# Performance work log

Measured on AMD Instinct MI355X. Metric: run time of the kernel, lower is better.

The kernel has to match this reference:

```python
import jax, jax.numpy as jnp
import numpy as np

D = 768; HID = 384; B = 256; T = 96
N_EMO = 128; N_CAU = 256; CK = 4; NK = N_CAU // CK; POS = 50
EPS_BN = 1e-5

def _lrelu(x):
    return jax.nn.leaky_relu(x, 0.01)

def _lstm(x, Wih, Whh, bih, bhh):
    # x: [B,T,D] -> hidden states [B,T,HID]; PyTorch gate order i,f,g,o
    h0 = jnp.zeros((x.shape[0], Whh.shape[1]), x.dtype)
    def step(carry, xt):
        h, c = carry
        g = xt @ Wih.T + bih + h @ Whh.T + bhh
        i, f, gg, o = jnp.split(g, 4, axis=-1)
        c = jax.nn.sigmoid(f) * c + jax.nn.sigmoid(i) * jnp.tanh(gg)
        h = jax.nn.sigmoid(o) * jnp.tanh(c)
        return (h, c), h
    _, hs = jax.lax.scan(step, (h0, h0), jnp.swapaxes(x, 0, 1))
    return jnp.swapaxes(hs, 0, 1)

def _item_att(E, Y):
    # E: [e,d], Y: [e,k,d] -> cat(x.repeat, y, ||x-y||, x*y) : [e,k,3d+1]
    Eb = jnp.broadcast_to(E[:, None, :], Y.shape)
    nrm = jnp.linalg.norm(Eb - Y, axis=-1, keepdims=True)
    return jnp.concatenate([Eb, Y, nrm, Eb * Y], axis=-1)

def _bn(x):
    # BatchNorm1d(affine=False, track_running_stats=False): batch stats, biased var
    m = x.mean(axis=1, keepdims=True)
    v = x.var(axis=1, keepdims=True)
    return (x - m) / jnp.sqrt(v + EPS_BN)

def setup_inputs() -> dict:
    key = jax.random.key(0)
    ks = jax.random.split(key, 26)
    s = 0.05
    g = lambda k, shp: (jax.random.normal(k, shp, jnp.float32) * s)
    inp = {
        'word_encode': jax.random.normal(ks[0], (B, T, D), jnp.float32),
        'pos_encode': jax.random.normal(ks[1], (N_EMO, NK, POS), jnp.float32),
        'dis_encode': jax.random.normal(ks[2], (1, N_CAU, POS), jnp.float32),
        'Wih_f': g(ks[3], (4 * HID, D)), 'Whh_f': g(ks[4], (4 * HID, HID)),
        'bih_f': g(ks[5], (4 * HID,)), 'bhh_f': g(ks[6], (4 * HID,)),
        'Wih_b': g(ks[7], (4 * HID, D)), 'Whh_b': g(ks[8], (4 * HID, HID)),
        'bih_b': g(ks[9], (4 * HID,)), 'bhh_b': g(ks[10], (4 * HID,)),
        's1_W': g(ks[11], (D, D)), 's1_b': g(ks[12], (D,)),
        's2_W': g(ks[13], (D, 1)),
        'rep_W': g(ks[14], (D, D)), 'rep_b': g(ks[15], (D,)),
        'W2_W': g(ks[16], (3 * D + 1 + POS, D)), 'W2_b': g(ks[17], (D,)),
        'Wo_W': g(ks[18], (D, 2)), 'Wo_b': g(ks[19], (2,)),
        'W3_W': g(ks[20], (3 * D + 2 + POS, D)), 'W3_b': g(ks[21], (D,)),
        'cls_W': g(ks[22], (D, 2)), 'cls_b': g(ks[23], (2,)),
        'sen_lengths': jax.random.randint(ks[24], (B,), T // 2, T + 1),
        'emo_idx': jnp.arange(N_EMO) * 2,
        'cau_idx': jnp.arange(N_CAU),
        'label3': jax.random.randint(ks[25], (N_EMO, 3), -1, N_CAU),
    }
    return inp

def reference(word_encode, pos_encode, dis_encode, Wih_f, Whh_f, bih_f, bhh_f,
              Wih_b, Whh_b, bih_b, bhh_b, s1_W, s1_b, s2_W, rep_W, rep_b,
              W2_W, W2_b, Wo_W, Wo_b, W3_W, W3_b, cls_W, cls_b,
              sen_lengths, emo_idx, cau_idx, label3):
    t = jnp.arange(T)
    # reverse-within-length index for the backward LSTM direction
    rev_idx = jnp.where(t[None, :] < sen_lengths[:, None],
                        sen_lengths[:, None] - 1 - t[None, :], t[None, :])
    hs_f = _lstm(word_encode, Wih_f, Whh_f, bih_f, bhh_f)
    x_rev = jnp.take_along_axis(word_encode, rev_idx[:, :, None], axis=1)
    hs_b = jnp.take_along_axis(_lstm(x_rev, Wih_b, Whh_b, bih_b, bhh_b),
                               rev_idx[:, :, None], axis=1)
    Hs = jnp.concatenate([hs_f, hs_b], axis=-1)  # [B,T,D]
    # att_var with softmax_by_length as written (mask*score / sum)
    e = (_lrelu(Hs @ s1_W + s1_b) @ s2_W)[..., 0]  # [B,T]
    mask = (t[None, :] < sen_lengths[:, None]).astype(Hs.dtype)
    num = e * mask
    alpha = num / (jnp.sum(num, axis=-1, keepdims=True) + 1e-9)
    U = jnp.einsum('bt,btd->bd', alpha, Hs)  # [B,D]
    # share_rep=True branch
    E = _lrelu(U[emo_idx] @ rep_W + rep_b)   # [n_emo,D]
    Cu = _lrelu(U[cau_idx] @ rep_W + rep_b)  # [n_cau,D]
    C = Cu.reshape(NK, CK, D)
    # per-chunk cross attention (softmax over chunk members)
    sc = jax.nn.softmax(jnp.einsum('ed,kcd->ekc', E, C), axis=-1)
    chunkEmb = jnp.einsum('ekc,kcd->ekd', sc, C)  # [e,NK,D]
    delta = jnp.concatenate([_item_att(E, chunkEmb), pos_encode], axis=-1)
    h2 = _lrelu(_bn(delta @ W2_W + W2_b))
    out2 = jax.nn.log_softmax(h2 @ Wo_W + Wo_b, axis=-1)  # [e,NK,2]
    out_feat = jax.lax.stop_gradient(jnp.argmax(out2, axis=-1).astype(Hs.dtype))
    # phase 3: all chunks selected (ck_mask all ones)
    delta_d = _item_att(E, jnp.broadcast_to(Cu[None], (N_EMO, N_CAU, D)))
    extra = jnp.repeat(out_feat, CK, axis=1)[..., None]  # [e,n_cau,1]
    dis = jnp.broadcast_to(dis_encode[0][None], (N_EMO, N_CAU, POS))
    delta3 = jnp.concatenate([delta_d, dis, extra], axis=-1)
    h3 = _lrelu(_bn(delta3 @ W3_W + W3_b))
    p = jax.nn.log_softmax(h3 @ cls_W + cls_b, axis=-1)  # [e,n_cau,2]
    # label3_out: L_cau indicator per emotion
    valid = (label3 >= 0)[..., None].astype(p.dtype)
    L = jnp.clip(jnp.sum(jax.nn.one_hot(label3, N_CAU, dtype=p.dtype) * valid,
                         axis=1), 0.0, 1.0)
    return out2, p, L
```

## Files before the change

kernel.cpp:

```cpp
#include <hip/hip_runtime.h>
#include <cstdint>
#include <cstddef>


#define DEV __device__ __forceinline__
typedef float f32x4 __attribute__((ext_vector_type(4)));
typedef __bf16 bf16;
typedef bf16 bf16x8 __attribute__((ext_vector_type(8)));

struct G32 {
    const float* A;
    const float* B;
    float* out;
    const float* bias;
    const float* s2v;
    float* escoreP;
    int M, N, K, lda, ldb, ldc;
};

template <int EPI>
__global__ __launch_bounds__(512) void k_gemm32(G32 p) {
    __shared__ __align__(16) float As[32][132];
    __shared__ __align__(16) float Bs[32][132];
    const int tid = threadIdx.x;
    const int tx = tid & 15, ty = tid >> 4;
    const int m0 = blockIdx.y * 128, n0 = blockIdx.x * 128;
    float acc[4][8] = {};
    const int ra = tid >> 2;
    const int ka = (tid & 3) * 8;

    const float* arow = p.A + (size_t)(m0 + ra) * p.lda;
    const float* brow = p.B + (size_t)(n0 + ra) * p.ldb;

    auto load_tile = [&](int kt, float* av, float* bv) {
        const float* ap = arow + kt + ka;
#pragma unroll
        for (int q = 0; q < 8; q++) av[q] = ap[q];
        const float* bp = brow + kt + ka;
#pragma unroll
        for (int q = 0; q < 8; q++) bv[q] = bp[q];
    };

    const int nt = p.K / 32;
    float av[8], bv[8];
    load_tile(0, av, bv);
    for (int t = 0; t < nt; t++) {
        __syncthreads();
#pragma unroll
        for (int q = 0; q < 8; q++) {
            As[ka + q][ra] = av[q];
            Bs[ka + q][ra] = bv[q];
        }
        __syncthreads();
        if (t + 1 < nt) load_tile((t + 1) * 32, av, bv);
#pragma unroll
        for (int kk = 0; kk < 32; kk++) {
            float a[4], b[8];
            *(f32x4*)a = *(const f32x4*)&As[kk][ty * 4];
            *(f32x4*)b = *(const f32x4*)&Bs[kk][tx * 4];
            *(f32x4*)(b + 4) = *(const f32x4*)&Bs[kk][64 + tx * 4];
#pragma unroll
            for (int i = 0; i < 4; i++)
#pragma unroll
                for (int j = 0; j < 8; j++) acc[i][j] += a[i] * b[j];
        }
    }

    if constexpr (EPI == 3) {
#pragma unroll
        for (int i = 0; i < 4; i++) {
            float s = 0.f;
#pragma unroll
            for (int j = 0; j < 8; j++) {
                int n = n0 + ((j < 4) ? tx * 4 + j : 64 + tx * 4 + (j - 4));
                float x = acc[i][j] + p.bias[n];
                x = x > 0.f ? x : 0.01f * x;
                s += x * p.s2v[n];
            }
            s += __shfl_xor(s, 1);
            s += __shfl_xor(s, 2);
            s += __shfl_xor(s, 4);
            s += __shfl_xor(s, 8);
            if (tx == 0) {
                int m = m0 + ty * 4 + i;
                p.escoreP[(size_t)m * 6 + blockIdx.x] = s;
            }
        }
    } else {
#pragma unroll
        for (int i = 0; i < 4; i++)
#pragma unroll
            for (int j = 0; j < 8; j++) {
                int m = m0 + ty * 4 + i;
                int n = n0 + ((j < 4) ? tx * 4 + j : 64 + tx * 4 + (j - 4));
                float x = acc[i][j];
                if constexpr (EPI == 0) {
                    if (p.bias) x += p.bias[n];
                } else if constexpr (EPI == 2) {
                    x += p.bias[n];
                    x = x > 0.f ? x : 0.01f * x;
                }
                p.out[(size_t)m * p.ldc + n] = x;
            }
    }
}

struct GSP {
    const float* srcA;
    const bf16* BH;
    const bf16* BL;
    float* out;
    const float* bias;
    const float* addE;
    const float* addB;
    const float* nrm;
    const float* wn;
    const float* feat;
    const float* wx;
    const float* ce;
    const float* CuEf;
    const float* pos;
    const int* slen;
    int K, ldb, ldc, c0;
};

template <int AMODE, int EPI>
__global__ __launch_bounds__(256) void k_gemm_sp(GSP p) {
    __shared__ __align__(16) bf16 AhS[128 * 32];
    __shared__ __align__(16) bf16 AlS[128 * 32];
    __shared__ __align__(16) bf16 BhS[128 * 32];
    __shared__ __align__(16) bf16 BlS[128 * 32];
    const int tid = threadIdx.x;
    const int lane = tid & 63;
    const int w = tid >> 6;
    const int wm = w >> 1, wn_ = w & 1;
    const int m0 = blockIdx.y * 128, n0 = blockIdx.x * 128;
    const int l15 = lane & 15, lq = lane >> 4;

    f32x4 zero4 = {0.f, 0.f, 0.f, 0.f};
    f32x4 acc[4][4];
#pragma unroll
    for (int i = 0; i < 4; i++)
#pragma unroll
        for (int j = 0; j < 4; j++) acc[i][j] = zero4;

    const int c0s = tid, c1s = tid + 256;
    const int ar0 = c0s >> 2, ao0 = (c0s & 3) << 3;
    const int ar1 = c1s >> 2, ao1 = (c1s & 3) << 3;
    const int gm0 = m0 + ar0, gm1 = m0 + ar1;

    const float* arow0 = nullptr;
    const float* arow1 = nullptr;
    const float *er0 = nullptr, *cr0 = nullptr, *pr0 = nullptr;
    const float *er1 = nullptr, *cr1 = nullptr, *pr1 = nullptr;
    if constexpr (AMODE == 1 || AMODE == 3) {
        int b0 = gm0 >> 5, t0 = p.c0 + (gm0 & 31);
        int b1 = gm1 >> 5, t1 = p.c0 + (gm1 & 31);
        if constexpr (AMODE == 3) {
            int len0 = p.slen[b0], len1 = p.slen[b1];
            t0 = (t0 < len0) ? len0 - 1 - t0 : t0;
            t1 = (t1 < len1) ? len1 - 1 - t1 : t1;
        }
        arow0 = p.srcA + ((size_t)b0 * 96 + t0) * 768;
        arow1 = p.srcA + ((size_t)b1 * 96 + t1) * 768;
    } else if constexpr (AMODE == 2) {
        er0 = p.CuEf + (size_t)(256 + (gm0 >> 8)) * 768;
        cr0 = p.CuEf + (size_t)(gm0 & 255) * 768;
        er1 = p.CuEf + (size_t)(256 + (gm1 >> 8)) * 768;
        cr1 = p.CuEf + (size_t)(gm1 & 255) * 768;
    } else {
        er0 = p.CuEf + (size_t)(256 + (gm0 >> 6)) * 768;
        cr0 = p.ce + (size_t)gm0 * 768;
        pr0 = p.pos + (size_t)gm0 * 50;
        er1 = p.CuEf + (size_t)(256 + (gm1 >> 6)) * 768;
        cr1 = p.ce + (size_t)gm1 * 768;
        pr1 = p.pos + (size_t)gm1 * 50;
    }
    const bf16* bh0 = p.BH + (size_t)(n0 + ar0) * p.ldb;
    const bf16* bl0 = p.BL + (size_t)(n0 + ar0) * p.ldb;
    const bf16* bh1 = p.BH + (size_t)(n0 + ar1) * p.ldb;
    const bf16* bl1 = p.BL + (size_t)(n0 + ar1) * p.ldb;

    auto loadA = [&](int kt, int ao, const float* arow, const float* er,
                     const float* cr, const float* pr, float* a) {
        if constexpr (AMODE == 1 || AMODE == 3) {
#pragma unroll
            for (int q = 0; q < 8; q++) a[q] = arow[kt + ao + q];
        } else if constexpr (AMODE == 2) {
#pragma unroll
            for (int q = 0; q < 8; q++) a[q] = er[kt + ao + q] * cr[kt + ao + q];
        } else {
#pragma unroll
            for (int q = 0; q < 8; q++) {
                int k = kt + ao + q;
                float v;
                if (k < 768) v = cr[k];
                else if (k < 1536) v = er[k - 768] * cr[k - 768];
                else if (k < 1586) v = pr[k - 1536];
                else v = 0.f;
                a[q] = v;
            }
        }
    };

    const int nt = p.K / 32;
    float a0f[8], a1f[8];
    bf16x8 b0h, b0l, b1h, b1l;
    auto load_tile = [&](int kt) {
        loadA(kt, ao0, arow0, er0, cr0, pr0, a0f);
        loadA(kt, ao1, arow1, er1, cr1, pr1, a1f);
        b0h = *(const bf16x8*)(bh0 + kt + ao0);
        b0l = *(const bf16x8*)(bl0 + kt + ao0);
        b1h = *(const bf16x8*)(bh1 + kt + ao1);
        b1l = *(const bf16x8*)(bl1 + kt + ao1);
    };

    load_tile(0);
    for (int t = 0; t < nt; t++) {
        __syncthreads();
        {
            bf16x8 h8, l8;
#pragma unroll
            for (int q = 0; q < 8; q++) {
                bf16 h = (bf16)a0f[q];
                h8[q] = h;
                l8[q] = (bf16)(a0f[q] - (float)h);
            }
            *(bf16x8*)(AhS + (c0s << 3)) = h8;
            *(bf16x8*)(AlS + (c0s << 3)) = l8;
#pragma unroll
            for (int q = 0; q < 8; q++) {
                bf16 h = (bf16)a1f[q];
                h8[q] = h;
                l8[q] = (bf16)(a1f[q] - (float)h);
            }
            *(bf16x8*)(AhS + (c1s << 3)) = h8;
            *(bf16x8*)(AlS + (c1s << 3)) = l8;
            *(bf16x8*)(BhS + (c0s << 3)) = b0h;
            *(bf16x8*)(BlS + (c0s << 3)) = b0l;
            *(bf16x8*)(BhS + (c1s << 3)) = b1h;
            *(bf16x8*)(BlS + (c1s << 3)) = b1l;
        }
        __syncthreads();
        if (t + 1 < nt) load_tile((t + 1) * 32);

        bf16x8 ah[4], bh[4], xl[4];
#pragma unroll
        for (int i = 0; i < 4; i++) {
            ah[i] = *(const bf16x8*)(AhS + (wm * 64 + i * 16 + l15) * 32 + (lq << 3));
            bh[i] = *(const bf16x8*)(BhS + (wn_ * 64 + i * 16 + l15) * 32 + (lq << 3));
        }
#pragma unroll
        for (int i = 0; i < 4; i++)
#pragma unroll
            for (int j = 0; j < 4; j++)
                acc[i][j] = __builtin_amdgcn_mfma_f32_16x16x32_bf16(ah[i], bh[j], acc[i][j], 0, 0, 0);
#pragma unroll
        for (int i = 0; i < 4; i++)
            xl[i] = *(const bf16x8*)(AlS + (wm * 64 + i * 16 + l15) * 32 + (lq << 3));
#pragma unroll
        for (int i = 0; i < 4; i++)
#pragma unroll
            for (int j = 0; j < 4; j++)
                acc[i][j] = __builtin_amdgcn_mfma_f32_16x16x32_bf16(xl[i], bh[j], acc[i][j], 0, 0, 0);
#pragma unroll
        for (int i = 0; i < 4; i++)
            xl[i] = *(const bf16x8*)(BlS + (wn_ * 64 + i * 16 + l15) * 32 + (lq << 3));
#pragma unroll
        for (int i = 0; i < 4; i++)
#pragma unroll
            for (int j = 0; j < 4; j++)
                acc[i][j] = __builtin_amdgcn_mfma_f32_16x16x32_bf16(ah[i], xl[j], acc[i][j], 0, 0, 0);
    }

#pragma unroll
    for (int i = 0; i < 4; i++)
#pragma unroll
        for (int j = 0; j < 4; j++)
#pragma unroll
            for (int r = 0; r < 4; r++) {
                int m = m0 + wm * 64 + i * 16 + (lq << 2) + r;
                int n = n0 + wn_ * 64 + j * 16 + l15;
                float v = acc[i][j][r];
                if constexpr (EPI == 1) {
                    v += p.bias[n];
                } else if constexpr (EPI == 4) {
                    int e = m >> 6;
                    v += p.addE[(size_t)e * 768 + n] + p.nrm[m] * p.wn[n] + p.bias[n];
                } else if constexpr (EPI == 5) {
                    int e = m >> 8, jj = m & 255;
                    float ex = p.feat[e * 64 + (jj >> 2)];
                    v += p.addE[(size_t)e * 768 + n] + p.addB[(size_t)jj * 768 + n] +
                         p.nrm[m] * p.wn[n] + ex * p.wx[n];
                }
                p.out[(size_t)m * p.ldc + n] = v;
            }
}

__global__ void k_wpack(const float* __restrict__ whh, float* __restrict__ wp) {
    int idx = blockIdx.x * 256 + threadIdx.x;
    if (idx < 384 * 1536) {
        int k = idx / 1536, rem = idx - k * 1536;
        int u = rem >> 2, g = rem & 3;
        wp[idx] = whh[(size_t)(g * 384 + u) * 384 + k];
    }
}

__global__ __launch_bounds__(384) void k_lstm_rows(
    const float* __restrict__ gchF, const float* __restrict__ gchB,
    const float* __restrict__ wpF, const float* __restrict__ wpB,
    float* __restrict__ hbuf, float* __restrict__ cbuf, float* __restrict__ Hs,
    const int* __restrict__ slen, int c0) {
    __shared__ __align__(16) float hlds[4][384];
    const int tid = threadIdx.x;
    const int dir = blockIdx.x & 1;
    const int r0 = (blockIdx.x >> 1) * 4;
    const float* gch = dir ? gchB : gchF;
    const float* wp = dir ? wpB : wpF;
    float* hb = hbuf + (size_t)dir * 98304;
    float* cb = cbuf + (size_t)dir * 98304;
    const int u = tid;

    {
        int r = tid / 96, c4 = (tid - r * 96) * 4;
        *(f32x4*)&hlds[r][c4] = *(const f32x4*)&hb[(size_t)(r0 + r) * 384 + c4];
    }
    float c_[4];
    int len_[4];
#pragma unroll
    for (int r = 0; r < 4; r++) {
        c_[r] = cb[(size_t)(r0 + r) * 384 + u];
        len_[r] = slen[r0 + r];
    }
    __syncthreads();

    const float* wpb = wp + (size_t)u * 4;
    for (int t = c0; t < c0 + 32; t++) {
        float acc[4][4] = {};
#pragma unroll 4
        for (int k = 0; k < 384; k++) {
            f32x4 wv = *(const f32x4*)(wpb + (size_t)k * 1536);
            float h0 = hlds[0][k], h1 = hlds[1][k];
            float h2 = hlds[2][k], h3 = hlds[3][k];
#pragma unroll
            for (int g = 0; g < 4; g++) {
                acc[0][g] += h0 * wv[g];
                acc[1][g] += h1 * wv[g];
                acc[2][g] += h2 * wv[g];
                acc[3][g] += h3 * wv[g];
            }
        }
        __syncthreads();
#pragma unroll
        for (int r = 0; r < 4; r++) {
            int bg = r0 + r;
            int len = len_[r];
            int tsrc = dir ? (t < len ? len - 1 - t : t) : t;
            const float* gp = gch + (((size_t)bg << 5) + (t & 31)) * 1536;
            float gi = acc[r][0] + gp[u];
            float gf = acc[r][1] + gp[384 + u];
            float gg2 = acc[r][2] + gp[768 + u];
            float go = acc[r][3] + gp[1152 + u];
            float si = 1.f / (1.f + __expf(-gi));
            float sf = 1.f / (1.f + __expf(-gf));
            float so = 1.f / (1.f + __expf(-go));
            float tg = tanhf(gg2);
            float cn = sf * c_[r] + si * tg;
            float hn = so * tanhf(cn);
            c_[r] = cn;
            hlds[r][u] = hn;
            int tpos = dir ? tsrc : t;
            Hs[((size_t)bg * 96 + tpos) * 768 + dir * 384 + u] = hn;
        }
        __syncthreads();
    }

    {
        int r = tid / 96, c4 = (tid - r * 96) * 4;
        *(f32x4*)&hb[(size_t)(r0 + r) * 384 + c4] = *(const f32x4*)&hlds[r][c4];
    }
#pragma unroll
    for (int r = 0; r < 4; r++) cb[(size_t)(r0 + r) * 384 + u] = c_[r];
}

__global__ void k_bias2(const float* a, const float* b, float* o, int n) {
    int i = blockIdx.x * 256 + threadIdx.x;
    if (i < n) o[i] = a[i] + b[i];
}

__global__ void k_splitw(const float* __restrict__ src, bf16* __restrict__ hi,
                         bf16* __restrict__ lo, int n) {
    int i = blockIdx.x * 256 + threadIdx.x;
    if (i < n) {
        float v = src[i];
        bf16 h = (bf16)v;
        hi[i] = h;
        lo[i] = (bf16)(v - (float)h);
    }
}

__global__ __launch_bounds__(256) void k_transp32(const float* __restrict__ src,
                                                  float* __restrict__ dst, int roff) {
    __shared__ float tile[32][33];
    int tx = threadIdx.x & 31, ty = threadIdx.x >> 5;
    int n0 = blockIdx.x * 32, k0 = blockIdx.y * 32;
#pragma unroll
    for (int r = ty; r < 32; r += 8)
        tile[r][tx] = src[(size_t)(roff + k0 + r) * 768 + n0 + tx];
    __syncthreads();
#pragma unroll
    for (int r = ty; r < 32; r += 8)
        dst[(size_t)(n0 + r) * 768 + k0 + tx] = tile[tx][r];
}

__global__ __launch_bounds__(256) void k_transp_sp(const float* __restrict__ src,
                                                   bf16* __restrict__ hi,
                                                   bf16* __restrict__ lo, int roff) {
    __shared__ float tile[32][33];
    int tx = threadIdx.x & 31, ty = threadIdx.x >> 5;
    int n0 = blockIdx.x * 32, k0 = blockIdx.y * 32;
#pragma unroll
    for (int r = ty; r < 32; r += 8)
        tile[r][tx] = src[(size_t)(roff + k0 + r) * 768 + n0 + tx];
    __syncthreads();
#pragma unroll
    for (int r = ty; r < 32; r += 8) {
        float v = tile[tx][r];
        bf16 h = (bf16)v;
        hi[(size_t)(n0 + r) * 768 + k0 + tx] = h;
        lo[(size_t)(n0 + r) * 768 + k0 + tx] = (bf16)(v - (float)h);
    }
}

__global__ __launch_bounds__(256) void k_b2cat_sp(const float* __restrict__ W2,
                                                  bf16* __restrict__ hi,
                                                  bf16* __restrict__ lo) {
    __shared__ float tile[32][33];
    int tx = threadIdx.x & 31, ty = threadIdx.x >> 5;
    int n0 = blockIdx.x * 32, k0 = blockIdx.y * 32;
#pragma unroll
    for (int r = ty; r < 32; r += 8) {
        int k = k0 + r;
        float v = 0.f;
        if (k < 1586) {
            int sr = (k < 768) ? 768 + k : 769 + k;
            v = W2[(size_t)sr * 768 + n0 + tx];
        }
        tile[r][tx] = v;
    }
    __syncthreads();
#pragma unroll
    for (int r = ty; r < 32; r += 8) {
        float v = tile[tx][r];
        bf16 h = (bf16)v;
        hi[(size_t)(n0 + r) * 1600 + k0 + tx] = h;
        lo[(size_t)(n0 + r) * 1600 + k0 + tx] = (bf16)(v - (float)h);
    }
}

__global__ __launch_bounds__(256) void k_alpha_u(const float* __restrict__ escoreP,
                                                 const float* __restrict__ Hs,
                                                 const int* __restrict__ slen,
                                                 float* __restrict__ U) {
    __shared__ float al[96];
    __shared__ float dsh;
    int b = blockIdx.x, tid = threadIdx.x;
    int len = slen[b];
    if (tid < 96) {
        const float* ep = escoreP + (size_t)(b * 96 + tid) * 6;
        float e = ep[0] + ep[1] + ep[2] + ep[3] + ep[4] + ep[5];
        al[tid] = (tid < len) ? e : 0.f;
    }
    __syncthreads();
    if (tid == 0) {
        float s = 0.f;
        for (int i = 0; i < 96; i++) s += al[i];
        dsh = 1.f / (s + 1e-9f);
    }
    __syncthreads();
    float dinv = dsh;
    for (int d = tid; d < 768; d += 256) {
        float acc = 0.f;
        const float* hp = Hs + (size_t)b * 96 * 768 + d;
        for (int tt = 0; tt < 96; tt++) acc += al[tt] * hp[(size_t)tt * 768];
        U[(size_t)b * 768 + d] = acc * dinv;
    }
}

__global__ void k_ucat(const float* __restrict__ U, const int* __restrict__ cau,
                       const int* __restrict__ emo, float* __restrict__ Ucat) {
    int i = blockIdx.x * 256 + threadIdx.x;
    if (i < 384 * 768) {
        int r = i / 768, d = i - r * 768;
        int src = (r < 256) ? cau[r] : emo[r - 256];
        Ucat[i] = U[(size_t)src * 768 + d];
    }
}

__global__ __launch_bounds__(256) void k_chunk_sc(const float* __restrict__ CuEf,
                                                  float* __restrict__ sc) {
    int m = blockIdx.x;
    int e = m >> 6, nk = m & 63;
    int tid = threadIdx.x, w = tid >> 6, lane = tid & 63;
    const float* Er = CuEf + (size_t)(256 + e) * 768;
    const float* Cr = CuEf + (size_t)(nk * 4 + w) * 768;
    float acc = 0.f;
    for (int q = lane; q < 768; q += 64) acc += Er[q] * Cr[q];
    for (int off = 32; off; off >>= 1) acc += __shfl_xor(acc, off);
    __shared__ float S[4];
    if (lane == 0) S[w] = acc;
    __syncthreads();
    if (tid == 0) {
        float mx = fmaxf(fmaxf(S[0], S[1]), fmaxf(S[2], S[3]));
        float e0 = expf(S[0] - mx), e1 = expf(S[1] - mx), e2 = expf(S[2] - mx),
              e3 = expf(S[3] - mx);
        float inv = 1.f / (e0 + e1 + e2 + e3);
        sc[4 * m] = e0 * inv; sc[4 * m + 1] = e1 * inv;
        sc[4 * m + 2] = e2 * inv; sc[4 * m + 3] = e3 * inv;
    }
}

__global__ void k_chunk_emb(const float* __restrict__ sc, const float* __restrict__ CuEf,
                            float* __restrict__ ce) {
    int i = blockIdx.x * 256 + threadIdx.x;
    if (i < 8192 * 768) {
        int m = i / 768, d = i - m * 768;
        int nk = m & 63;
        const float* base = CuEf + (size_t)(nk * 4) * 768 + d;
        ce[i] = sc[4 * m] * base[0] + sc[4 * m + 1] * base[768] +
                sc[4 * m + 2] * base[1536] + sc[4 * m + 3] * base[2304];
    }
}

__global__ __launch_bounds__(256) void k_nrm2(const float* __restrict__ ce,
                                              const float* __restrict__ CuEf,
                                              float* __restrict__ nrm2) {
    int m = blockIdx.x, tid = threadIdx.x;
    int e = m >> 6;
    const float* cr = ce + (size_t)m * 768;
    const float* er = CuEf + (size_t)(256 + e) * 768;
    float ss = 0.f;
    for (int d = tid; d < 768; d += 256) {
        float df = er[d] - cr[d];
        ss += df * df;
    }
    for (int off = 32; off; off >>= 1) ss += __shfl_xor(ss, off);
    __shared__ float red[4];
    if ((tid & 63) == 0) red[tid >> 6] = ss;
    __syncthreads();
    if (tid == 0) nrm2[m] = sqrtf(red[0] + red[1] + red[2] + red[3]);
}

__global__ __launch_bounds__(256) void k_nrm3(const float* __restrict__ CuEf,
                                              float* __restrict__ nrm3) {
    int m = blockIdx.x, tid = threadIdx.x;
    int e = m >> 8, j = m & 255;
    const float* cu = CuEf + (size_t)j * 768;
    const float* er = CuEf + (size_t)(256 + e) * 768;
    float ss = 0.f;
    for (int d = tid; d < 768; d += 256) {
        float df = er[d] - cu[d];
        ss += df * df;
    }
    for (int off = 32; off; off >>= 1) ss += __shfl_xor(ss, off);
    __shared__ float red[4];
    if ((tid & 63) == 0) red[tid >> 6] = ss;
    __syncthreads();
    if (tid == 0) nrm3[m] = sqrtf(red[0] + red[1] + red[2] + red[3]);
}

__global__ void k_bv3_dis(float* __restrict__ Bv3, const float* __restrict__ dis,
                          const float* __restrict__ W3, const float* __restrict__ b3) {
    int i = blockIdx.x * 256 + threadIdx.x;
    if (i < 256 * 768) {
        int j = i / 768, n = i - j * 768;
        float s = Bv3[i] + b3[n];
        const float* dr = dis + j * 50;
#pragma unroll 10
        for (int q = 0; q < 50; q++) s += dr[q] * W3[(size_t)(2305 + q) * 768 + n];
        Bv3[i] = s;
    }
}

template <int GROUP>
__global__ __launch_bounds__(256) void k_bnstats(const float* __restrict__ z,
                                                 float* __restrict__ mean,
                                                 float* __restrict__ rstd) {
    int idx = blockIdx.x * 256 + threadIdx.x;
    if (idx >= 128 * 768) return;
    int e = idx / 768, n = idx - e * 768;
    const float* p = z + (size_t)e * GROUP * 768 + n;
    float s = 0.f;
    for (int k = 0; k < GROUP; k++) s += p[(size_t)k * 768];
    float mu = s * (1.f / GROUP);
    float q = 0.f;
    for (int k = 0; k < GROUP; k++) {
        float d = p[(size_t)k * 768] - mu;
        q += d * d;
    }
    mean[idx] = mu;
    rstd[idx] = rsqrtf(q * (1.f / GROUP) + 1e-5f);
}

template <int GROUP>
__global__ __launch_bounds__(256) void k_bn_head(const float* __restrict__ z,
                                                 const float* __restrict__ mean,
                                                 const float* __restrict__ rstd,
                                                 const float* __restrict__ W,
                                                 const float* __restrict__ bb,
                                                 float* __restrict__ outp,
                                                 float* __restrict__ feat) {
    int m = blockIdx.x;
    int e = m / GROUP;
    int tid = threadIdx.x;
    float a0 = 0.f, a1 = 0.f;
    const float* zr = z + (size_t)m * 768;
    const float* mr = mean + (size_t)e * 768;
    const float* rr = rstd + (size_t)e * 768;
    for (int n = tid; n < 768; n += 256) {
        float h = (zr[n] - mr[n]) * rr[n];
        h = h > 0.f ? h : 0.01f * h;
        a0 += h * W[2 * n];
        a1 += h * W[2 * n + 1];
    }
    for (int off = 32; off; off >>= 1) {
        a0 += __shfl_xor(a0, off);
        a1 += __shfl_xor(a1, off);
    }
    __shared__ float s0[4], s1v[4];
    int w = tid >> 6;
    if ((tid & 63) == 0) { s0[w] = a0; s1v[w] = a1; }
    __syncthreads();
    if (tid == 0) {
        float l0 = s0[0] + s0[1] + s0[2] + s0[3] + bb[0];
        float l1 = s1v[0] + s1v[1] + s1v[2] + s1v[3] + bb[1];
        float mx = fmaxf(l0, l1);
        float ls = mx + logf(expf(l0 - mx) + expf(l1 - mx));
        outp[2 * m] = l0 - ls;
        outp[2 * m + 1] = l1 - ls;
        if (feat) feat[m] = (l1 > l0) ? 1.f : 0.f;
    }
}

__global__ void k_label(const int* __restrict__ l3, float* __restrict__ out) {
    int e = blockIdx.x, c = threadIdx.x;
    int a = l3[e * 3], b = l3[e * 3 + 1], d = l3[e * 3 + 2];
    out[e * 256 + c] = (a == c || b == c || d == c) ? 1.f : 0.f;
}

extern "C" void kernel_launch(void* const* d_in, const int* in_sizes, int n_in,
                              void* d_out, int out_size, void* d_ws, size_t ws_size,
                              hipStream_t stream) {
    (void)in_sizes; (void)n_in; (void)out_size; (void)ws_size;
    const float* word = (const float*)d_in[0];
    const float* pos = (const float*)d_in[1];
    const float* dis = (const float*)d_in[2];
    const float* WihF = (const float*)d_in[3];
    const float* WhhF = (const float*)d_in[4];
    const float* bihF = (const float*)d_in[5];
    const float* bhhF = (const float*)d_in[6];
    const float* WihB = (const float*)d_in[7];
    const float* WhhB = (const float*)d_in[8];
    const float* bihB = (const float*)d_in[9];
    const float* bhhB = (const float*)d_in[10];
    const float* s1W = (const float*)d_in[11];
    const float* s1b = (const float*)d_in[12];
    const float* s2W = (const float*)d_in[13];
    const float* repW = (const float*)d_in[14];
    const float* repb = (const float*)d_in[15];
    const float* W2W = (const float*)d_in[16];
    const float* W2b = (const float*)d_in[17];
    const float* WoW = (const float*)d_in[18];
    const float* Wob = (const float*)d_in[19];
    const float* W3W = (const float*)d_in[20];
    const float* W3b = (const float*)d_in[21];
    const float* clsW = (const float*)d_in[22];
    const float* clsb = (const float*)d_in[23];
    const int* slen = (const int*)d_in[24];
    const int* emo = (const int*)d_in[25];
    const int* cau = (const int*)d_in[26];
    const int* lab3 = (const int*)d_in[27];
    float* out = (float*)d_out;

    char* ws = (char*)d_ws;
    size_t off = 0;
    auto alloc = [&](size_t b) -> char* {
        char* p = ws + off;
        off += (b + 255) & ~(size_t)255;
        return p;
    };
    float* biasF = (float*)alloc(1536 * 4);
    float* biasB = (float*)alloc(1536 * 4);
    float* wpF = (float*)alloc((size_t)384 * 1536 * 4);
    float* wpB = (float*)alloc((size_t)384 * 1536 * 4);
    bf16* wihFH = (bf16*)alloc((size_t)1536 * 768 * 2);
    bf16* wihFL = (bf16*)alloc((size_t)1536 * 768 * 2);
    bf16* wihBH = (bf16*)alloc((size_t)1536 * 768 * 2);
    bf16* wihBL = (bf16*)alloc((size_t)1536 * 768 * 2);
    bf16* B2H = (bf16*)alloc((size_t)768 * 1600 * 2);
    bf16* B2L = (bf16*)alloc((size_t)768 * 1600 * 2);
    bf16* W3dH = (bf16*)alloc((size_t)768 * 768 * 2);
    bf16* W3dL = (bf16*)alloc((size_t)768 * 768 * 2);
    float* s1T = (float*)alloc((size_t)768 * 768 * 4);
    float* repT = (float*)alloc((size_t)768 * 768 * 4);
    float* W2aT = (float*)alloc((size_t)768 * 768 * 4);
    float* W3aT = (float*)alloc((size_t)768 * 768 * 4);
    float* W3bT = (float*)alloc((size_t)768 * 768 * 4);
    float* hbuf = (float*)alloc((size_t)2 * 98304 * 4);
    float* cbuf = (float*)alloc((size_t)2 * 98304 * 4);
    float* Hsf = (float*)alloc((size_t)24576 * 768 * 4);
    float* escoreP = (float*)alloc((size_t)24576 * 6 * 4);
    float* Uf = (float*)alloc((size_t)256 * 768 * 4);
    float* UcatF = (float*)alloc((size_t)384 * 768 * 4);
    float* CuEf = (float*)alloc((size_t)384 * 768 * 4);
    float* scF = (float*)alloc((size_t)8192 * 4 * 4);
    float* nrm2F = (float*)alloc(8192 * 4);
    float* nrm3F = (float*)alloc(32768 * 4);
    float* E2F = (float*)alloc((size_t)128 * 768 * 4);
    float* E3F = (float*)alloc((size_t)128 * 768 * 4);
    float* Bv3F = (float*)alloc((size_t)256 * 768 * 4);
    float* mean2 = (float*)alloc((size_t)128 * 768 * 4);
    float* rstd2 = (float*)alloc((size_t)128 * 768 * 4);
    float* mean3 = (float*)alloc((size_t)128 * 768 * 4);
    float* rstd3 = (float*)alloc((size_t)128 * 768 * 4);
    float* outfeatF = (float*)alloc(8192 * 4);
    char* BIG = alloc((size_t)103 * 1024 * 1024);

    float* gchF = (float*)BIG;
    float* gchB = (float*)(BIG + (size_t)50331648);
    float* ceF = (float*)BIG;
    float* z2F = (float*)(BIG + (size_t)25165824);
    float* z3F = (float*)BIG;

    hipMemsetAsync(hbuf, 0, (size_t)4 * 98304 * 4, stream);

    k_bias2<<<6, 256, 0, stream>>>(bihF, bhhF, biasF, 1536);
    k_bias2<<<6, 256, 0, stream>>>(bihB, bhhB, biasB, 1536);
    k_wpack<<<2304, 256, 0, stream>>>(WhhF, wpF);
    k_wpack<<<2304, 256, 0, stream>>>(WhhB, wpB);
    k_splitw<<<4608, 256, 0, stream>>>(WihF, wihFH, wihFL, 1536 * 768);
    k_splitw<<<4608, 256, 0, stream>>>(WihB, wihBH, wihBL, 1536 * 768);
    k_transp32<<<dim3(24, 24), 256, 0, stream>>>(s1W, s1T, 0);
    k_transp32<<<dim3(24, 24), 256, 0, stream>>>(repW, repT, 0);
    k_transp32<<<dim3(24, 24), 256, 0, stream>>>(W2W, W2aT, 0);
    k_transp32<<<dim3(24, 24), 256, 0, stream>>>(W3W, W3aT, 0);
    k_transp32<<<dim3(24, 24), 256, 0, stream>>>(W3W, W3bT, 768);
    k_transp_sp<<<dim3(24, 24), 256, 0, stream>>>(W3W, W3dH, W3dL, 1537);
    k_b2cat_sp<<<dim3(24, 50), 256, 0, stream>>>(W2W, B2H, B2L);

    for (int c = 0; c < 3; c++) {
        {
            GSP g{};
            g.srcA = word; g.BH = wihFH; g.BL = wihFL; g.out = gchF;
            g.bias = biasF; g.slen = slen;
            g.K = 768; g.ldb = 768; g.ldc = 1536; g.c0 = c * 32;
            k_gemm_sp<1, 1><<<dim3(12, 64), 256, 0, stream>>>(g);
            g.BH = wihBH; g.BL = wihBL; g.bias = biasB; g.out = gchB;
            k_gemm_sp<3, 1><<<dim3(12, 64), 256, 0, stream>>>(g);
        }
        k_lstm_rows<<<128, 384, 0, stream>>>(gchF, gchB, wpF, wpB,
                                             hbuf, cbuf, Hsf, slen, c * 32);
    }

    {
        G32 g{};
        g.A = Hsf; g.B = s1T; g.bias = s1b; g.s2v = s2W; g.escoreP = escoreP;
        g.M = 24576; g.N = 768; g.K = 768; g.lda = 768; g.ldb = 768; g.ldc = 768;
        k_gemm32<3><<<dim3(6, 192), 512, 0, stream>>>(g);
    }
    k_alpha_u<<<256, 256, 0, stream>>>(escoreP, Hsf, slen, Uf);
    k_ucat<<<(384 * 768 + 255) / 256, 256, 0, stream>>>(Uf, cau, emo, UcatF);

    {
        G32 g{};
        g.A = UcatF; g.B = repT; g.bias = repb; g.out = CuEf;
        g.M = 384; g.N = 768; g.K = 768; g.lda = 768; g.ldb = 768; g.ldc = 768;
        k_gemm32<2><<<dim3(6, 3), 512, 0, stream>>>(g);
    }

    k_chunk_sc<<<8192, 256, 0, stream>>>(CuEf, scF);
    k_chunk_emb<<<(8192 * 768 + 255) / 256, 256, 0, stream>>>(scF, CuEf, ceF);

    k_nrm2<<<8192, 256, 0, stream>>>(ceF, CuEf, nrm2F);
    {
        G32 g{};
        g.A = CuEf + (size_t)256 * 768; g.B = W2aT; g.out = E2F;
        g.M = 128; g.N = 768; g.K = 768; g.lda = 768; g.ldb = 768; g.ldc = 768;
        k_gemm32<0><<<dim3(6, 1), 512, 0, stream>>>(g);
    }
    {
        GSP g{};
        g.BH = B2H; g.BL = B2L; g.out = z2F; g.bias = W2b;
        g.addE = E2F; g.nrm = nrm2F; g.wn = W2W + (size_t)1536 * 768;
        g.ce = ceF; g.CuEf = CuEf; g.pos = pos;
        g.K = 1600; g.ldb = 1600; g.ldc = 768;
        k_gemm_sp<4, 4><<<dim3(6, 64), 256, 0, stream>>>(g);
    }
    k_bnstats<64><<<384, 256, 0, stream>>>(z2F, mean2, rstd2);
    k_bn_head<64><<<8192, 256, 0, stream>>>(z2F, mean2, rstd2, WoW, Wob, out, outfeatF);

    k_nrm3<<<32768, 256, 0, stream>>>(CuEf, nrm3F);
    {
        G32 g{};
        g.A = CuEf; g.B = W3bT; g.out = Bv3F;
        g.M = 256; g.N = 768; g.K = 768; g.lda = 768; g.ldb = 768; g.ldc = 768;
        k_gemm32<0><<<dim3(6, 2), 512, 0, stream>>>(g);
    }
    k_bv3_dis<<<(256 * 768 + 255) / 256, 256, 0, stream>>>(Bv3F, dis, W3W, W3b);
    {
        G32 g{};
        g.A = CuEf + (size_t)256 * 768; g.B = W3aT; g.out = E3F;
        g.M = 128; g.N = 768; g.K = 768; g.lda = 768; g.ldb = 768; g.ldc = 768;
        k_gemm32<0><<<dim3(6, 1), 512, 0, stream>>>(g);
    }
    {
        GSP g{};
        g.BH = W3dH; g.BL = W3dL; g.out = z3F;
        g.addE = E3F; g.addB = Bv3F; g.nrm = nrm3F; g.wn = W3W + (size_t)1536 * 768;
        g.feat = outfeatF; g.wx = W3W + (size_t)2355 * 768;
        g.CuEf = CuEf;
        g.K = 768; g.ldb = 768; g.ldc = 768;
        k_gemm_sp<2, 5><<<dim3(6, 256), 256, 0, stream>>>(g);
    }
    k_bnstats<256><<<384, 256, 0, stream>>>(z3F, mean3, rstd3);
    k_bn_head<256><<<32768, 256, 0, stream>>>(z3F, mean3, rstd3, clsW, clsb, out + 16384, nullptr);

    k_label<<<128, 256, 0, stream>>>(lab3, out + 81920);
}
```

Measured before the change: 4.102 ms.

## Move attention score GEMM to split-bf16 MFMA and prefetch LSTM recurrent weights

The large Hsf×s1 attention-score GEMM (24576×768×768) moves from the FP32 SIMT GEMM to the split-bf16 (hi/lo) MFMA kernel. A fused LeakyReLU and s2 dot-product epilogue writes 12 partial scores per row, which k_alpha_u now sums. Separately, the LSTM recurrent loop double-buffers its weight vector loads in registers to hide global latency. The split-bf16 scheme approximates FP32 with three MFMA products, and the extra prefetch registers may lower occupancy in the LSTM kernel.

```diff
diff --git a/kernel.cpp b/kernel.cpp
--- a/kernel.cpp
+++ b/kernel.cpp
@@ -13,8 +13,6 @@
     const float* B;
     float* out;
     const float* bias;
-    const float* s2v;
-    float* escoreP;
     int M, N, K, lda, ldb, ldc;
 };
 
@@ -66,43 +64,21 @@
         }
     }
 
-    if constexpr (EPI == 3) {
-#pragma unroll
-        for (int i = 0; i < 4; i++) {
-            float s = 0.f;
-#pragma unroll
-            for (int j = 0; j < 8; j++) {
-                int n = n0 + ((j < 4) ? tx * 4 + j : 64 + tx * 4 + (j - 4));
-                float x = acc[i][j] + p.bias[n];
+#pragma unroll
+    for (int i = 0; i < 4; i++)
+#pragma unroll
+        for (int j = 0; j < 8; j++) {
+            int m = m0 + ty * 4 + i;
+            int n = n0 + ((j < 4) ? tx * 4 + j : 64 + tx * 4 + (j - 4));
+            float x = acc[i][j];
+            if constexpr (EPI == 0) {
+                if (p.bias) x += p.bias[n];
+            } else if constexpr (EPI == 2) {
+                x += p.bias[n];
                 x = x > 0.f ? x : 0.01f * x;
-                s += x * p.s2v[n];
             }
-            s += __shfl_xor(s, 1);
-            s += __shfl_xor(s, 2);
-            s += __shfl_xor(s, 4);
-            s += __shfl_xor(s, 8);
-            if (tx == 0) {
-                int m = m0 + ty * 4 + i;
-                p.escoreP[(size_t)m * 6 + blockIdx.x] = s;
-            }
-        }
-    } else {
-#pragma unroll
-        for (int i = 0; i < 4; i++)
-#pragma unroll
-            for (int j = 0; j < 8; j++) {
-                int m = m0 + ty * 4 + i;
-                int n = n0 + ((j < 4) ? tx * 4 + j : 64 + tx * 4 + (j - 4));
-                float x = acc[i][j];
-                if constexpr (EPI == 0) {
-                    if (p.bias) x += p.bias[n];
-                } else if constexpr (EPI == 2) {
-                    x += p.bias[n];
-                    x = x > 0.f ? x : 0.01f * x;
-                }
-                p.out[(size_t)m * p.ldc + n] = x;
-            }
-    }
+            p.out[(size_t)m * p.ldc + n] = x;
+        }
 }
 
 struct GSP {
@@ -111,6 +87,8 @@
     const bf16* BL;
     float* out;
     const float* bias;
+    const float* s2v;
+    float* escoreP;
     const float* addE;
     const float* addB;
     const float* nrm;
@@ -153,7 +131,10 @@
     const float* arow1 = nullptr;
     const float *er0 = nullptr, *cr0 = nullptr, *pr0 = nullptr;
     const float *er1 = nullptr, *cr1 = nullptr, *pr1 = nullptr;
-    if constexpr (AMODE == 1 || AMODE == 3) {
+    if constexpr (AMODE == 0) {
+        arow0 = p.srcA + (size_t)gm0 * 768;
+        arow1 = p.srcA + (size_t)gm1 * 768;
+    } else if constexpr (AMODE == 1 || AMODE == 3) {
         int b0 = gm0 >> 5, t0 = p.c0 + (gm0 & 31);
         int b1 = gm1 >> 5, t1 = p.c0 + (gm1 & 31);
         if constexpr (AMODE == 3) {
@@ -183,7 +164,7 @@
 
     auto loadA = [&](int kt, int ao, const float* arow, const float* er,
                      const float* cr, const float* pr, float* a) {
-        if constexpr (AMODE == 1 || AMODE == 3) {
+        if constexpr (AMODE == 0 || AMODE == 1 || AMODE == 3) {
 #pragma unroll
             for (int q = 0; q < 8; q++) a[q] = arow[kt + ao + q];
         } else if constexpr (AMODE == 2) {
@@ -273,28 +254,52 @@
                 acc[i][j] = __builtin_amdgcn_mfma_f32_16x16x32_bf16(ah[i], xl[j], acc[i][j], 0, 0, 0);
     }
 
-#pragma unroll
-    for (int i = 0; i < 4; i++)
-#pragma unroll
-        for (int j = 0; j < 4; j++)
+    if constexpr (EPI == 3) {
+#pragma unroll
+        for (int i = 0; i < 4; i++)
 #pragma unroll
             for (int r = 0; r < 4; r++) {
-                int m = m0 + wm * 64 + i * 16 + (lq << 2) + r;
-                int n = n0 + wn_ * 64 + j * 16 + l15;
-                float v = acc[i][j][r];
-                if constexpr (EPI == 1) {
-                    v += p.bias[n];
-                } else if constexpr (EPI == 4) {
-                    int e = m >> 6;
-                    v += p.addE[(size_t)e * 768 + n] + p.nrm[m] * p.wn[n] + p.bias[n];
-                } else if constexpr (EPI == 5) {
-                    int e = m >> 8, jj = m & 255;
-                    float ex = p.feat[e * 64 + (jj >> 2)];
-                    v += p.addE[(size_t)e * 768 + n] + p.addB[(size_t)jj * 768 + n] +
-                         p.nrm[m] * p.wn[n] + ex * p.wx[n];
+                float s = 0.f;
+#pragma unroll
+                for (int j = 0; j < 4; j++) {
+                    int n = n0 + wn_ * 64 + j * 16 + l15;
+                    float v = acc[i][j][r] + p.bias[n];
+                    v = v > 0.f ? v : 0.01f * v;
+                    s += v * p.s2v[n];
                 }
-                p.out[(size_t)m * p.ldc + n] = v;
+                s += __shfl_xor(s, 1);
+                s += __shfl_xor(s, 2);
+                s += __shfl_xor(s, 4);
+                s += __shfl_xor(s, 8);
+                if (l15 == 0) {
+                    int m = m0 + wm * 64 + i * 16 + (lq << 2) + r;
+                    p.escoreP[(size_t)m * 12 + blockIdx.x * 2 + wn_] = s;
+                }
             }
+    } else {
+#pragma unroll
+        for (int i = 0; i < 4; i++)
+#pragma unroll
+            for (int j = 0; j < 4; j++)
+#pragma unroll
+                for (int r = 0; r < 4; r++) {
+                    int m = m0 + wm * 64 + i * 16 + (lq << 2) + r;
+                    int n = n0 + wn_ * 64 + j * 16 + l15;
+                    float v = acc[i][j][r];
+                    if constexpr (EPI == 1) {
+                        v += p.bias[n];
+                    } else if constexpr (EPI == 4) {
+                        int e = m >> 6;
+                        v += p.addE[(size_t)e * 768 + n] + p.nrm[m] * p.wn[n] + p.bias[n];
+                    } else if constexpr (EPI == 5) {
+                        int e = m >> 8, jj = m & 255;
+                        float ex = p.feat[e * 64 + (jj >> 2)];
+                        v += p.addE[(size_t)e * 768 + n] + p.addB[(size_t)jj * 768 + n] +
+                             p.nrm[m] * p.wn[n] + ex * p.wx[n];
+                    }
+                    p.out[(size_t)m * p.ldc + n] = v;
+                }
+    }
 }
 
 __global__ void k_wpack(const float* __restrict__ whh, float* __restrict__ wp) {
@@ -337,18 +342,31 @@
     const float* wpb = wp + (size_t)u * 4;
     for (int t = c0; t < c0 + 32; t++) {
         float acc[4][4] = {};
-#pragma unroll 4
-        for (int k = 0; k < 384; k++) {
-            f32x4 wv = *(const f32x4*)(wpb + (size_t)k * 1536);
-            float h0 = hlds[0][k], h1 = hlds[1][k];
-            float h2 = hlds[2][k], h3 = hlds[3][k];
-#pragma unroll
-            for (int g = 0; g < 4; g++) {
-                acc[0][g] += h0 * wv[g];
-                acc[1][g] += h1 * wv[g];
-                acc[2][g] += h2 * wv[g];
-                acc[3][g] += h3 * wv[g];
+        f32x4 wa[4], wb[4];
+#pragma unroll
+        for (int q = 0; q < 4; q++) wa[q] = *(const f32x4*)(wpb + (size_t)q * 1536);
+        for (int k0 = 0; k0 < 384; k0 += 4) {
+            if (k0 + 4 < 384) {
+#pragma unroll
+                for (int q = 0; q < 4; q++)
+                    wb[q] = *(const f32x4*)(wpb + (size_t)(k0 + 4 + q) * 1536);
             }
+#pragma unroll
+            for (int q = 0; q < 4; q++) {
+                int k = k0 + q;
+                f32x4 wv = wa[q];
+                float h0 = hlds[0][k], h1 = hlds[1][k];
+                float h2 = hlds[2][k], h3 = hlds[3][k];
+#pragma unroll
+                for (int g = 0; g < 4; g++) {
+                    acc[0][g] += h0 * wv[g];
+                    acc[1][g] += h1 * wv[g];
+                    acc[2][g] += h2 * wv[g];
+                    acc[3][g] += h3 * wv[g];
+                }
+            }
+#pragma unroll
+            for (int q = 0; q < 4; q++) wa[q] = wb[q];
         }
         __syncthreads();
 #pragma unroll
@@ -467,8 +485,10 @@
     int b = blockIdx.x, tid = threadIdx.x;
     int len = slen[b];
     if (tid < 96) {
-        const float* ep = escoreP + (size_t)(b * 96 + tid) * 6;
-        float e = ep[0] + ep[1] + ep[2] + ep[3] + ep[4] + ep[5];
+        const float* ep = escoreP + (size_t)(b * 96 + tid) * 12;
+        float e = 0.f;
+#pragma unroll
+        for (int q = 0; q < 12; q++) e += ep[q];
         al[tid] = (tid < len) ? e : 0.f;
     }
     __syncthreads();
@@ -697,11 +717,12 @@
     bf16* wihFL = (bf16*)alloc((size_t)1536 * 768 * 2);
     bf16* wihBH = (bf16*)alloc((size_t)1536 * 768 * 2);
     bf16* wihBL = (bf16*)alloc((size_t)1536 * 768 * 2);
+    bf16* s1H = (bf16*)alloc((size_t)768 * 768 * 2);
+    bf16* s1L = (bf16*)alloc((size_t)768 * 768 * 2);
     bf16* B2H = (bf16*)alloc((size_t)768 * 1600 * 2);
     bf16* B2L = (bf16*)alloc((size_t)768 * 1600 * 2);
     bf16* W3dH = (bf16*)alloc((size_t)768 * 768 * 2);
     bf16* W3dL = (bf16*)alloc((size_t)768 * 768 * 2);
-    float* s1T = (float*)alloc((size_t)768 * 768 * 4);
     float* repT = (float*)alloc((size_t)768 * 768 * 4);
     float* W2aT = (float*)alloc((size_t)768 * 768 * 4);
     float* W3aT = (float*)alloc((size_t)768 * 768 * 4);
@@ -709,7 +730,7 @@
     float* hbuf = (float*)alloc((size_t)2 * 98304 * 4);
     float* cbuf = (float*)alloc((size_t)2 * 98304 * 4);
     float* Hsf = (float*)alloc((size_t)24576 * 768 * 4);
-    float* escoreP = (float*)alloc((size_t)24576 * 6 * 4);
+    float* escoreP = (float*)alloc((size_t)24576 * 12 * 4);
     float* Uf = (float*)alloc((size_t)256 * 768 * 4);
     float* UcatF = (float*)alloc((size_t)384 * 768 * 4);
     float* CuEf = (float*)alloc((size_t)384 * 768 * 4);
@@ -740,7 +761,7 @@
     k_wpack<<<2304, 256, 0, stream>>>(WhhB, wpB);
     k_splitw<<<4608, 256, 0, stream>>>(WihF, wihFH, wihFL, 1536 * 768);
     k_splitw<<<4608, 256, 0, stream>>>(WihB, wihBH, wihBL, 1536 * 768);
-    k_transp32<<<dim3(24, 24), 256, 0, stream>>>(s1W, s1T, 0);
+    k_transp_sp<<<dim3(24, 24), 256, 0, stream>>>(s1W, s1H, s1L, 0);
     k_transp32<<<dim3(24, 24), 256, 0, stream>>>(repW, repT, 0);
     k_transp32<<<dim3(24, 24), 256, 0, stream>>>(W2W, W2aT, 0);
     k_transp32<<<dim3(24, 24), 256, 0, stream>>>(W3W, W3aT, 0);
@@ -763,10 +784,11 @@
     }
 
     {
-        G32 g{};
-        g.A = Hsf; g.B = s1T; g.bias = s1b; g.s2v = s2W; g.escoreP = escoreP;
-        g.M = 24576; g.N = 768; g.K = 768; g.lda = 768; g.ldb = 768; g.ldc = 768;
-        k_gemm32<3><<<dim3(6, 192), 512, 0, stream>>>(g);
+        GSP g{};
+        g.srcA = Hsf; g.BH = s1H; g.BL = s1L; g.bias = s1b; g.s2v = s2W;
+        g.escoreP = escoreP;
+        g.K = 768; g.ldb = 768; g.ldc = 768; g.c0 = 0;
+        k_gemm_sp<0, 3><<<dim3(6, 192), 256, 0, stream>>>(g);
     }
     k_alpha_u<<<256, 256, 0, stream>>>(escoreP, Hsf, slen, Uf);
     k_ucat<<<(384 * 768 + 255) / 256, 256, 0, stream>>>(Uf, cau, emo, UcatF);
```

Measured after the change: 4.177 ms. No clear change (+1.8%).
